# Kernel optimization log

Hardware: AMD Instinct MI355X
Metric: run time of the kernel (lower is better)

The kernel has to match this reference:

```python
import jax, jax.numpy as jnp
import numpy as np

B, H, W, C, NH, WS, SHIFT = 32, 56, 56, 128, 4, 7, 3
N = WS * WS            # tokens per window = 49
HD = C // NH           # head dim = 32
HID = int(C * 4.0)     # mlp hidden = 512
SCALE = HD ** -0.5
EPS = 1e-5


def _rel_index():
    coords = np.stack(np.meshgrid(np.arange(WS), np.arange(WS), indexing='ij')).reshape(2, -1)
    rel = (coords[:, :, None] - coords[:, None, :]).transpose(1, 2, 0).copy()
    rel[:, :, 0] += WS - 1
    rel[:, :, 1] += WS - 1
    rel[:, :, 0] *= 2 * WS - 1
    return jnp.asarray(rel.sum(-1), jnp.int32)  # [N, N]


def setup_inputs() -> dict:
    key = jax.random.key(0)
    ks = jax.random.split(key, 8)
    n = lambda k, s, std=0.02: jax.random.normal(k, s, jnp.float32) * std
    return {
        'x': jax.random.normal(ks[0], (B, H * W, C), jnp.float32),
        'attn_mask': jnp.zeros(((H // WS) * (W // WS), N, N), jnp.float32),  # unused (source bug)
        'norm1_w': jnp.ones((C,), jnp.float32), 'norm1_b': jnp.zeros((C,), jnp.float32),
        'qkv_w': n(ks[1], (3 * C, C)), 'qkv_b': jnp.zeros((3 * C,), jnp.float32),
        'rel_table': n(ks[2], ((2 * WS - 1) ** 2, NH)),
        'rel_index': _rel_index(),
        'proj_w': n(ks[3], (C, C)), 'proj_b': jnp.zeros((C,), jnp.float32),
        'norm2_w': jnp.ones((C,), jnp.float32), 'norm2_b': jnp.zeros((C,), jnp.float32),
        'fc1_w': n(ks[4], (HID, C)), 'fc1_b': jnp.zeros((HID,), jnp.float32),
        'fc2_w': n(ks[5], (C, HID)), 'fc2_b': jnp.zeros((C,), jnp.float32),
    }


def _ln(x, w, b):
    m = x.mean(-1, keepdims=True)
    v = jnp.mean((x - m) ** 2, -1, keepdims=True)
    return (x - m) * jax.lax.rsqrt(v + EPS) * w + b


def reference(x, attn_mask, norm1_w, norm1_b, qkv_w, qkv_b, rel_table, rel_index,
              proj_w, proj_b, norm2_w, norm2_b, fc1_w, fc1_b, fc2_w, fc2_b):
    # NOTE: attn_mask is accepted but never used by the source WindowAttention (faithful).
    shortcut = x
    h = _ln(x, norm1_w, norm1_b).reshape(B, H, W, C)
    # cyclic shift (shift_size > 0)
    h = jnp.roll(h, (-SHIFT, -SHIFT), axis=(1, 2))
    # window partition -> [B*nW, N, C]
    h = h.reshape(B, H // WS, WS, W // WS, WS, C).transpose(0, 1, 3, 2, 4, 5).reshape(-1, N, C)
    # window attention
    qkv = (h @ qkv_w.T + qkv_b).reshape(-1, N, 3, NH, HD)
    q = qkv[:, :, 0].transpose(0, 2, 1, 3)  # [BW, NH, N, HD]
    k = qkv[:, :, 1].transpose(0, 2, 1, 3)
    v = qkv[:, :, 2].transpose(0, 2, 1, 3)
    attn = jnp.einsum('whnd,whmd->whnm', q, k) * SCALE  # [BW, NH, N, N]
    bias = rel_table[rel_index.reshape(-1)].reshape(N, N, NH).transpose(2, 0, 1)
    attn = jax.nn.softmax(attn + bias[None], axis=-1)
    out = jnp.einsum('whnm,whmd->whnd', attn, v).transpose(0, 2, 1, 3).reshape(-1, N, C)
    out = out @ proj_w.T + proj_b
    # window reverse -> [B, H, W, C]
    out = out.reshape(B, H // WS, W // WS, WS, WS, C).transpose(0, 1, 3, 2, 4, 5).reshape(B, H, W, C)
    out = jnp.roll(out, (SHIFT, SHIFT), axis=(1, 2)).reshape(B, H * W, C)
    y = shortcut + out
    # MLP block
    h2 = _ln(y, norm2_w, norm2_b)
    h2 = jax.nn.gelu(h2 @ fc1_w.T + fc1_b, approximate=False)
    h2 = h2 @ fc2_w.T + fc2_b
    return y + h2
```

## Files before the change

### kernel.cpp

```cpp
#include <hip/hip_runtime.h>

typedef __bf16 bf16;
typedef __bf16 bf16x4 __attribute__((ext_vector_type(4)));
typedef __bf16 bf16x8 __attribute__((ext_vector_type(8)));
typedef float f32x4 __attribute__((ext_vector_type(4)));

#define NTOK 49
#define HW 56
#define SHIFT3 3
constexpr float kScale = 0.17677669529663687f;

#define WS_BIAS  0
#define WS_QKVW  50176
#define WS_PROJW 148480
#define WS_FC1W  181248
#define WS_FC2W  312320

static __device__ __forceinline__ f32x4 mfma16(bf16x8 a, bf16x8 b, f32x4 c) {
    return __builtin_amdgcn_mfma_f32_16x16x32_bf16(a, b, c, 0, 0, 0);
}

static __device__ __forceinline__ float gelu_f(float x) {
    float x2 = x * x;
    float u2 = x * (1.5957691216f + 0.0713548162f * x2);
    return x / (1.0f + __expf(-u2));
}


__global__ void bias_kernel(const float* __restrict__ rel_table,
                            const int* __restrict__ rel_index,
                            float* __restrict__ biasbuf) {
    int idx = blockIdx.x * 256 + threadIdx.x;
    if (idx >= 4 * NTOK * 64) return;
    int j = idx & 63;
    int rest = idx >> 6;
    int i = rest % NTOK;
    int h = rest / NTOK;
    float v = -1e30f;
    if (j < NTOK) v = rel_table[rel_index[i * NTOK + j] * 4 + h];
    biasbuf[idx] = v;
}

__global__ void wcvt_kernel(const float* __restrict__ qkv_w, const float* __restrict__ proj_w,
                            const float* __restrict__ fc1_w, const float* __restrict__ fc2_w,
                            bf16* __restrict__ qkvwp, bf16* __restrict__ projwp,
                            bf16* __restrict__ fc1wp, bf16* __restrict__ fc2wp) {
    int idx = blockIdx.x * 256 + threadIdx.x;
    if (idx < 49152) {
        int o = idx, e = o & 7, t = o >> 3, g = t & 3; t >>= 2;
        int row = t % 384, ks = t / 384;
        qkvwp[o] = (bf16)qkv_w[row * 128 + ks * 32 + g * 8 + e];
    } else if (idx < 65536) {
        int o = idx - 49152, e = o & 7, t = o >> 3, g = t & 3; t >>= 2;
        int row = t % 128, ks = t / 128;
        projwp[o] = (bf16)proj_w[row * 128 + ks * 32 + g * 8 + e];
    } else if (idx < 131072) {
        int o = idx - 65536, e = o & 7, t = o >> 3, g = t & 3; t >>= 2;
        int row = t % 512, ks = t / 512;
        fc1wp[o] = (bf16)fc1_w[row * 128 + ks * 32 + g * 8 + e];
    } else {
        int o = idx - 131072, e = o & 7, t = o >> 3, g = t & 3; t >>= 2;
        int row = t % 128, ks = t / 128;
        fc2wp[o] = (bf16)fc2_w[row * 512 + ks * 32 + g * 8 + e];
    }
}


__global__ __launch_bounds__(256, 3) void attn_kernel(
    const float* __restrict__ x,
    const float* __restrict__ n1w, const float* __restrict__ n1b,
    const bf16*  __restrict__ qkvwp, const float* __restrict__ qkv_b,
    const bf16*  __restrict__ projwp, const float* __restrict__ proj_b,
    const float* __restrict__ biasbuf,
    float* __restrict__ yout)
{
    __shared__ __align__(16) char smem[49152];
    bf16* const hb = (bf16*)smem;

    const int tid  = threadIdx.x;
    const int wave = tid >> 6;
    const int lane = tid & 63;
    const int g = lane >> 4;
    const int c = lane & 15;

    char* const qbase  = smem + 16384 + wave * 8192;
    char* const kbase  = qbase + 4096;
    char* const pbase  = qbase;
    char* const vtbase = smem + wave * 4096;

    const int w  = blockIdx.x;
    const int b  = w >> 6;
    const int wi = (w >> 3) & 7;
    const int wj = w & 7;
    const int head = wave;

    {
        const int slot = tid >> 5, l32 = tid & 31;
        for (int it = 0; it < 8; ++it) {
            int t  = slot + (it << 3);
            int tt = t < NTOK ? t : NTOK - 1;
            int r  = tt / 7, cc = tt - r * 7;
            int row = wi * 7 + r + SHIFT3;  if (row >= HW) row -= HW;
            int col = wj * 7 + cc + SHIFT3; if (col >= HW) col -= HW;
            const float* src = x + (((size_t)(b * 3136 + row * 56 + col)) << 7) + (l32 << 2);
            float4 v = *(const float4*)src;
            float s  = v.x + v.y + v.z + v.w;
            float s2 = v.x * v.x + v.y * v.y + v.z * v.z + v.w * v.w;
            for (int m = 1; m <= 16; m <<= 1) {
                s  += __shfl_xor(s,  m, 64);
                s2 += __shfl_xor(s2, m, 64);
            }
            float mean = s * (1.0f / 128.0f);
            float var  = s2 * (1.0f / 128.0f) - mean * mean;
            float rs   = rsqrtf(var + 1e-5f);
            float4 wv = *(const float4*)(n1w + (l32 << 2));
            float4 bv = *(const float4*)(n1b + (l32 << 2));
            bf16x4 outv;
            if (t < NTOK) {
                outv[0] = (bf16)((v.x - mean) * rs * wv.x + bv.x);
                outv[1] = (bf16)((v.y - mean) * rs * wv.y + bv.y);
                outv[2] = (bf16)((v.z - mean) * rs * wv.z + bv.z);
                outv[3] = (bf16)((v.w - mean) * rs * wv.w + bv.w);
            } else {
                outv[0] = (bf16)0.0f; outv[1] = (bf16)0.0f;
                outv[2] = (bf16)0.0f; outv[3] = (bf16)0.0f;
            }
            int off = (l32 << 3) ^ ((t & 7) << 4);
            *(bf16x4*)((char*)hb + t * 256 + off) = outv;
        }
    }
    __syncthreads();

    f32x4 fz = {0.f, 0.f, 0.f, 0.f};
    f32x4 va[2][4];
    #pragma unroll
    for (int nt = 0; nt < 2; ++nt) {
        f32x4 qa[4], ka[4];
        #pragma unroll
        for (int mt = 0; mt < 4; ++mt) { qa[mt] = fz; ka[mt] = fz; va[nt][mt] = fz; }

        #pragma unroll
        for (int ks = 0; ks < 4; ++ks) {
            bf16x8 af[4];
            const int koff = ks * 64 + g * 16;
            #pragma unroll
            for (int mt = 0; mt < 4; ++mt) {
                int row = mt * 16 + c;
                af[mt] = *(const bf16x8*)((char*)hb + row * 256 + (koff ^ ((row & 7) << 4)));
            }
            int jb = head * 32 + nt * 16 + c;
            bf16x8 bq = *(const bf16x8*)(qkvwp + (((ks * 384 + jb) * 4 + g) << 3));
            bf16x8 bk = *(const bf16x8*)(qkvwp + (((ks * 384 + 128 + jb) * 4 + g) << 3));
            bf16x8 bv = *(const bf16x8*)(qkvwp + (((ks * 384 + 256 + jb) * 4 + g) << 3));
            #pragma unroll
            for (int mt = 0; mt < 4; ++mt) {
                qa[mt] = mfma16(bq, af[mt], qa[mt]);
                ka[mt] = mfma16(bk, af[mt], ka[mt]);
                va[nt][mt] = mfma16(af[mt], bv, va[nt][mt]);
            }
        }
        f32x4 qb4 = *(const f32x4*)(qkv_b + head * 32 + nt * 16 + g * 4);
        f32x4 kb4 = *(const f32x4*)(qkv_b + 128 + head * 32 + nt * 16 + g * 4);
        #pragma unroll
        for (int mt = 0; mt < 4; ++mt) {
            int tok = mt * 16 + c;
            bf16x4 qv, kv;
            #pragma unroll
            for (int r = 0; r < 4; ++r) {
                qv[r] = (bf16)(qa[mt][r] + qb4[r]);
                kv[r] = (bf16)(ka[mt][r] + kb4[r]);
            }
            int qoff = (nt * 32 + g * 8) ^ ((tok & 3) << 4);
            *(bf16x4*)(qbase + tok * 64 + qoff) = qv;
            *(bf16x4*)(kbase + tok * 64 + qoff) = kv;
        }
    }
    __syncthreads();

    #pragma unroll
    for (int nt = 0; nt < 2; ++nt) {
        float vb = qkv_b[256 + head * 32 + nt * 16 + c];
        int dl = nt * 16 + c;
        #pragma unroll
        for (int mt = 0; mt < 4; ++mt) {
            bf16x4 vv;
            #pragma unroll
            for (int r = 0; r < 4; ++r) vv[r] = (bf16)(va[nt][mt][r] + vb);
            *(bf16x4*)(vtbase + dl * 128 + ((mt * 32 + g * 8) ^ ((dl & 7) << 4))) = vv;
        }
    }

    f32x4 s[4][4];
    #pragma unroll
    for (int bm = 0; bm < 4; ++bm) for (int bn = 0; bn < 4; ++bn) s[bm][bn] = fz;
    {
        bf16x8 aq[4];
        #pragma unroll
        for (int bm = 0; bm < 4; ++bm) {
            int row = bm * 16 + c;
            aq[bm] = *(const bf16x8*)(qbase + row * 64 + ((g * 16) ^ ((row & 3) << 4)));
        }
        #pragma unroll
        for (int bn = 0; bn < 4; ++bn) {
            int row = bn * 16 + c;
            bf16x8 kf = *(const bf16x8*)(kbase + row * 64 + ((g * 16) ^ ((row & 3) << 4)));
            #pragma unroll
            for (int bm = 0; bm < 4; ++bm) s[bm][bn] = mfma16(kf, aq[bm], s[bm][bn]);
        }
    }

    const float* bbase = biasbuf + head * (NTOK * 64);
    float linv[4];
    #pragma unroll
    for (int bm = 0; bm < 4; ++bm) {
        int qt = bm * 16 + c;
        int im = qt < NTOK ? qt : NTOK - 1;
        const float* brow = bbase + im * 64;
        f32x4 vals[4];
        float mx = -3e38f;
        #pragma unroll
        for (int bn = 0; bn < 4; ++bn) {
            f32x4 b4 = *(const f32x4*)(brow + bn * 16 + g * 4);
            #pragma unroll
            for (int r = 0; r < 4; ++r) {
                float v = s[bm][bn][r] * kScale + b4[r];
                vals[bn][r] = v;
                mx = fmaxf(mx, v);
            }
        }
        mx = fmaxf(mx, __shfl_xor(mx, 16, 64));
        mx = fmaxf(mx, __shfl_xor(mx, 32, 64));
        float sum = 0.f;
        #pragma unroll
        for (int bn = 0; bn < 4; ++bn) {
            bf16x4 pv;
            #pragma unroll
            for (int r = 0; r < 4; ++r) {
                float p = __expf(vals[bn][r] - mx);
                sum += p;
                pv[r] = (bf16)p;
            }
            *(bf16x4*)(pbase + qt * 128 + ((bn * 32 + g * 8) ^ ((c & 7) << 4))) = pv;
        }
        sum += __shfl_xor(sum, 16, 64);
        sum += __shfl_xor(sum, 32, 64);
        linv[bm] = 1.0f / sum;
    }

    f32x4 o[4][2];
    #pragma unroll
    for (int mt = 0; mt < 4; ++mt) for (int nt = 0; nt < 2; ++nt) o[mt][nt] = fz;
    #pragma unroll
    for (int ks = 0; ks < 2; ++ks) {
        int koff = ks * 64 + g * 16;
        bf16x8 vf[2], pf[4];
        #pragma unroll
        for (int nt = 0; nt < 2; ++nt)
            vf[nt] = *(const bf16x8*)(vtbase + (nt * 16 + c) * 128 + (koff ^ ((c & 7) << 4)));
        #pragma unroll
        for (int mt = 0; mt < 4; ++mt)
            pf[mt] = *(const bf16x8*)(pbase + (mt * 16 + c) * 128 + (koff ^ ((c & 7) << 4)));
        #pragma unroll
        for (int mt = 0; mt < 4; ++mt)
            #pragma unroll
            for (int nt = 0; nt < 2; ++nt) o[mt][nt] = mfma16(vf[nt], pf[mt], o[mt][nt]);
    }
    __syncthreads();

    #pragma unroll
    for (int mt = 0; mt < 4; ++mt) {
        int qt = mt * 16 + c;
        if (qt < NTOK) {
            float inv = linv[mt];
            #pragma unroll
            for (int nt = 0; nt < 2; ++nt) {
                bf16x4 ov;
                #pragma unroll
                for (int r = 0; r < 4; ++r) ov[r] = (bf16)(o[mt][nt][r] * inv);
                int coff = (head * 64 + nt * 32 + g * 8) ^ ((qt & 7) << 4);
                *(bf16x4*)((char*)hb + qt * 256 + coff) = ov;
            }
        }
    }
    __syncthreads();

    f32x4 pj[4][2];
    #pragma unroll
    for (int mt = 0; mt < 4; ++mt) for (int nt = 0; nt < 2; ++nt) pj[mt][nt] = fz;
    #pragma unroll
    for (int ks = 0; ks < 4; ++ks) {
        bf16x8 af[4];
        int koff = ks * 64 + g * 16;
        #pragma unroll
        for (int mt = 0; mt < 4; ++mt) {
            int row = mt * 16 + c;
            af[mt] = *(const bf16x8*)((char*)hb + row * 256 + (koff ^ ((row & 7) << 4)));
        }
        #pragma unroll
        for (int nt = 0; nt < 2; ++nt) {
            int colw = wave * 32 + nt * 16 + c;
            bf16x8 bp = *(const bf16x8*)(projwp + (((ks * 128 + colw) * 4 + g) << 3));
            #pragma unroll
            for (int mt = 0; mt < 4; ++mt) pj[mt][nt] = mfma16(bp, af[mt], pj[mt][nt]);
        }
    }
    f32x4 pb0 = *(const f32x4*)(proj_b + wave * 32 + g * 4);
    f32x4 pb1 = *(const f32x4*)(proj_b + wave * 32 + 16 + g * 4);
    #pragma unroll
    for (int mt = 0; mt < 4; ++mt) {
        int qt = mt * 16 + c;
        if (qt < NTOK) {
            int rr = qt / 7, cc = qt - rr * 7;
            int row = wi * 7 + rr + SHIFT3;  if (row >= HW) row -= HW;
            int col = wj * 7 + cc + SHIFT3;  if (col >= HW) col -= HW;
            size_t base = ((size_t)(b * 3136 + row * 56 + col)) << 7;
            int c0 = wave * 32 + g * 4;
            f32x4 x0 = *(const f32x4*)(x + base + c0);
            f32x4 x1 = *(const f32x4*)(x + base + c0 + 16);
            f32x4 y0 = x0 + pj[mt][0] + pb0;
            f32x4 y1 = x1 + pj[mt][1] + pb1;
            *(f32x4*)(yout + base + c0)      = y0;
            *(f32x4*)(yout + base + c0 + 16) = y1;
        }
    }
}


__global__ __launch_bounds__(256, 5) void mlp_kernel(
    const float* __restrict__ n2w, const float* __restrict__ n2b,
    const bf16*  __restrict__ fc1wp, const float* __restrict__ fc1_b,
    const bf16*  __restrict__ fc2wp, const float* __restrict__ fc2_b,
    float* __restrict__ y)
{
    __shared__ __align__(16) char smem[32768];
    bf16* const h2    = (bf16*)smem;
    char* const abase = smem;

    const int tid  = threadIdx.x;
    const int wave = tid >> 6;
    const int lane = tid & 63;
    const int g = lane >> 4;
    const int c = lane & 15;
    const size_t t0 = (size_t)blockIdx.x * 32;

    {
        const int slot = tid >> 5, l32 = tid & 31;
        for (int it = 0; it < 4; ++it) {
            int t = slot + (it << 3);
            const float* src = y + ((t0 + t) << 7) + (l32 << 2);
            float4 v = *(const float4*)src;
            float s  = v.x + v.y + v.z + v.w;
            float s2 = v.x * v.x + v.y * v.y + v.z * v.z + v.w * v.w;
            for (int m = 1; m <= 16; m <<= 1) {
                s  += __shfl_xor(s,  m, 64);
                s2 += __shfl_xor(s2, m, 64);
            }
            float mean = s * (1.0f / 128.0f);
            float var  = s2 * (1.0f / 128.0f) - mean * mean;
            float rs   = rsqrtf(var + 1e-5f);
            float4 wv = *(const float4*)(n2w + (l32 << 2));
            float4 bv = *(const float4*)(n2b + (l32 << 2));
            bf16x4 outv;
            outv[0] = (bf16)((v.x - mean) * rs * wv.x + bv.x);
            outv[1] = (bf16)((v.y - mean) * rs * wv.y + bv.y);
            outv[2] = (bf16)((v.z - mean) * rs * wv.z + bv.z);
            outv[3] = (bf16)((v.w - mean) * rs * wv.w + bv.w);
            int off = (l32 << 3) ^ ((t & 7) << 4);
            *(bf16x4*)((char*)h2 + t * 256 + off) = outv;
        }
    }
    __syncthreads();

    f32x4 fz = {0.f, 0.f, 0.f, 0.f};
    f32x4 a1[8][2];
    #pragma unroll
    for (int nt = 0; nt < 8; ++nt) for (int mt = 0; mt < 2; ++mt) a1[nt][mt] = fz;
    #pragma unroll
    for (int ks = 0; ks < 4; ++ks) {
        bf16x8 af[2];
        int koff = ks * 64 + g * 16;
        #pragma unroll
        for (int mt = 0; mt < 2; ++mt) {
            int row = mt * 16 + c;
            af[mt] = *(const bf16x8*)((char*)h2 + row * 256 + (koff ^ ((row & 7) << 4)));
        }
        #pragma unroll
        for (int nt = 0; nt < 8; ++nt) {
            int col = wave * 128 + nt * 16 + c;
            bf16x8 bw = *(const bf16x8*)(fc1wp + (((ks * 512 + col) * 4 + g) << 3));
            #pragma unroll
            for (int mt = 0; mt < 2; ++mt) a1[nt][mt] = mfma16(bw, af[mt], a1[nt][mt]);
        }
    }
    __syncthreads();

    #pragma unroll
    for (int nt = 0; nt < 8; ++nt) {
        f32x4 fb4 = *(const f32x4*)(fc1_b + wave * 128 + nt * 16 + g * 4);
        #pragma unroll
        for (int mt = 0; mt < 2; ++mt) {
            int tok = mt * 16 + c;
            bf16x4 gv;
            #pragma unroll
            for (int r = 0; r < 4; ++r) gv[r] = (bf16)gelu_f(a1[nt][mt][r] + fb4[r]);
            int coff = (wave * 256 + nt * 32 + g * 8) ^ ((tok & 7) << 4);
            *(bf16x4*)(abase + tok * 1024 + coff) = gv;
        }
    }
    __syncthreads();

    f32x4 a2[2][2];
    #pragma unroll
    for (int nt = 0; nt < 2; ++nt) for (int mt = 0; mt < 2; ++mt) a2[nt][mt] = fz;
    #pragma unroll 4
    for (int ks = 0; ks < 16; ++ks) {
        bf16x8 af[2];
        int koff = ks * 64 + g * 16;
        #pragma unroll
        for (int mt = 0; mt < 2; ++mt) {
            int row = mt * 16 + c;
            af[mt] = *(const bf16x8*)(abase + row * 1024 + (koff ^ ((row & 7) << 4)));
        }
        #pragma unroll
        for (int nt = 0; nt < 2; ++nt) {
            int col = wave * 32 + nt * 16 + c;
            bf16x8 bw = *(const bf16x8*)(fc2wp + (((ks * 128 + col) * 4 + g) << 3));
            #pragma unroll
            for (int mt = 0; mt < 2; ++mt) a2[nt][mt] = mfma16(bw, af[mt], a2[nt][mt]);
        }
    }
    #pragma unroll
    for (int nt = 0; nt < 2; ++nt) {
        f32x4 fb4 = *(const f32x4*)(fc2_b + wave * 32 + nt * 16 + g * 4);
        #pragma unroll
        for (int mt = 0; mt < 2; ++mt) {
            size_t idx = ((t0 + mt * 16 + c) << 7) + wave * 32 + nt * 16 + g * 4;
            f32x4 yv = *(const f32x4*)(y + idx);
            yv = yv + a2[nt][mt] + fb4;
            *(f32x4*)(y + idx) = yv;
        }
    }
}


extern "C" void kernel_launch(void* const* d_in, const int* in_sizes, int n_in,
                              void* d_out, int out_size, void* d_ws, size_t ws_size,
                              hipStream_t stream) {
    const float* x        = (const float*)d_in[0];
    const float* n1w      = (const float*)d_in[2];
    const float* n1b      = (const float*)d_in[3];
    const float* qkv_w    = (const float*)d_in[4];
    const float* qkv_b    = (const float*)d_in[5];
    const float* rel_tab  = (const float*)d_in[6];
    const int*   rel_idx  = (const int*)d_in[7];
    const float* proj_w   = (const float*)d_in[8];
    const float* proj_b   = (const float*)d_in[9];
    const float* n2w      = (const float*)d_in[10];
    const float* n2b      = (const float*)d_in[11];
    const float* fc1_w    = (const float*)d_in[12];
    const float* fc1_b    = (const float*)d_in[13];
    const float* fc2_w    = (const float*)d_in[14];
    const float* fc2_b    = (const float*)d_in[15];

    float* yout = (float*)d_out;
    char*  ws   = (char*)d_ws;
    float* biasbuf = (float*)(ws + WS_BIAS);
    bf16*  qkvwp = (bf16*)(ws + WS_QKVW);
    bf16*  projwp= (bf16*)(ws + WS_PROJW);
    bf16*  fc1wp = (bf16*)(ws + WS_FC1W);
    bf16*  fc2wp = (bf16*)(ws + WS_FC2W);

    bias_kernel<<<dim3(49), dim3(256), 0, stream>>>(rel_tab, rel_idx, biasbuf);
    wcvt_kernel<<<dim3(768), dim3(256), 0, stream>>>(qkv_w, proj_w, fc1_w, fc2_w,
                                                     qkvwp, projwp, fc1wp, fc2wp);
    attn_kernel<<<dim3(2048), dim3(256), 0, stream>>>(x, n1w, n1b, qkvwp, qkv_b,
                                                      projwp, proj_b, biasbuf, yout);
    mlp_kernel<<<dim3(3136), dim3(256), 0, stream>>>(n2w, n2b, fc1wp, fc1_b,
                                                     fc2wp, fc2_b, yout);
}
```

Measured before the change: 279.7 us.

## Fuse MLP block into window-attention kernel, keeping residual in registers

Merges the MLP kernel into the attention kernel. The post-projection residual stays in registers, LayerNorm2 is done with a cross-wave reduction through shared memory, and fc1/GELU/fc2 run in two hidden-dimension chunks that reuse shared memory. This removes the fp32 y round trip through global memory and one kernel launch. In exchange the fused kernel has higher register pressure, extra barriers, and M-tiles padded to 64 rows for 49 tokens, which wastes MFMA work in the MLP.

```diff
diff --git a/kernel.cpp b/kernel.cpp
--- a/kernel.cpp
+++ b/kernel.cpp
@@ -66,12 +66,15 @@
 }
 
 
-__global__ __launch_bounds__(256, 3) void attn_kernel(
+__global__ __launch_bounds__(256, 3) void attn_mlp_kernel(
     const float* __restrict__ x,
     const float* __restrict__ n1w, const float* __restrict__ n1b,
     const bf16*  __restrict__ qkvwp, const float* __restrict__ qkv_b,
     const bf16*  __restrict__ projwp, const float* __restrict__ proj_b,
     const float* __restrict__ biasbuf,
+    const float* __restrict__ n2w, const float* __restrict__ n2b,
+    const bf16*  __restrict__ fc1wp, const float* __restrict__ fc1_b,
+    const bf16*  __restrict__ fc2wp, const float* __restrict__ fc2_b,
     float* __restrict__ yout)
 {
     __shared__ __align__(16) char smem[49152];
@@ -87,6 +90,7 @@
     char* const kbase  = qbase + 4096;
     char* const pbase  = qbase;
     char* const vtbase = smem + wave * 4096;
+    char* const abase  = smem + 16384;
 
     const int w  = blockIdx.x;
     const int b  = w >> 6;
@@ -306,6 +310,7 @@
     }
     f32x4 pb0 = *(const f32x4*)(proj_b + wave * 32 + g * 4);
     f32x4 pb1 = *(const f32x4*)(proj_b + wave * 32 + 16 + g * 4);
+    f32x4 yreg[4][2];
     #pragma unroll
     for (int mt = 0; mt < 4; ++mt) {
         int qt = mt * 16 + c;
@@ -317,127 +322,144 @@
             int c0 = wave * 32 + g * 4;
             f32x4 x0 = *(const f32x4*)(x + base + c0);
             f32x4 x1 = *(const f32x4*)(x + base + c0 + 16);
-            f32x4 y0 = x0 + pj[mt][0] + pb0;
-            f32x4 y1 = x1 + pj[mt][1] + pb1;
-            *(f32x4*)(yout + base + c0)      = y0;
-            *(f32x4*)(yout + base + c0 + 16) = y1;
-        }
-    }
-}
-
-
-__global__ __launch_bounds__(256, 5) void mlp_kernel(
-    const float* __restrict__ n2w, const float* __restrict__ n2b,
-    const bf16*  __restrict__ fc1wp, const float* __restrict__ fc1_b,
-    const bf16*  __restrict__ fc2wp, const float* __restrict__ fc2_b,
-    float* __restrict__ y)
-{
-    __shared__ __align__(16) char smem[32768];
-    bf16* const h2    = (bf16*)smem;
-    char* const abase = smem;
-
-    const int tid  = threadIdx.x;
-    const int wave = tid >> 6;
-    const int lane = tid & 63;
-    const int g = lane >> 4;
-    const int c = lane & 15;
-    const size_t t0 = (size_t)blockIdx.x * 32;
+            yreg[mt][0] = x0 + pj[mt][0] + pb0;
+            yreg[mt][1] = x1 + pj[mt][1] + pb1;
+        } else {
+            yreg[mt][0] = fz; yreg[mt][1] = fz;
+        }
+    }
 
     {
-        const int slot = tid >> 5, l32 = tid & 31;
-        for (int it = 0; it < 4; ++it) {
-            int t = slot + (it << 3);
-            const float* src = y + ((t0 + t) << 7) + (l32 << 2);
-            float4 v = *(const float4*)src;
-            float s  = v.x + v.y + v.z + v.w;
-            float s2 = v.x * v.x + v.y * v.y + v.z * v.z + v.w * v.w;
-            for (int m = 1; m <= 16; m <<= 1) {
-                s  += __shfl_xor(s,  m, 64);
-                s2 += __shfl_xor(s2, m, 64);
-            }
-            float mean = s * (1.0f / 128.0f);
-            float var  = s2 * (1.0f / 128.0f) - mean * mean;
-            float rs   = rsqrtf(var + 1e-5f);
-            float4 wv = *(const float4*)(n2w + (l32 << 2));
-            float4 bv = *(const float4*)(n2b + (l32 << 2));
-            bf16x4 outv;
-            outv[0] = (bf16)((v.x - mean) * rs * wv.x + bv.x);
-            outv[1] = (bf16)((v.y - mean) * rs * wv.y + bv.y);
-            outv[2] = (bf16)((v.z - mean) * rs * wv.z + bv.z);
-            outv[3] = (bf16)((v.w - mean) * rs * wv.w + bv.w);
-            int off = (l32 << 3) ^ ((t & 7) << 4);
-            *(bf16x4*)((char*)h2 + t * 256 + off) = outv;
+        float* ssum = (float*)(smem + 16384);
+        float* ssq  = (float*)(smem + 16384 + 1024);
+        float lns[4], lnq[4];
+        #pragma unroll
+        for (int mt = 0; mt < 4; ++mt) {
+            float ps = 0.f, pq = 0.f;
+            #pragma unroll
+            for (int nt = 0; nt < 2; ++nt)
+                #pragma unroll
+                for (int r = 0; r < 4; ++r) {
+                    float v = yreg[mt][nt][r];
+                    ps += v; pq += v * v;
+                }
+            ps += __shfl_xor(ps, 16, 64);  pq += __shfl_xor(pq, 16, 64);
+            ps += __shfl_xor(ps, 32, 64);  pq += __shfl_xor(pq, 32, 64);
+            lns[mt] = ps; lnq[mt] = pq;
+        }
+        if (g == 0) {
+            #pragma unroll
+            for (int mt = 0; mt < 4; ++mt) {
+                int tok = mt * 16 + c;
+                ssum[tok * 4 + wave] = lns[mt];
+                ssq [tok * 4 + wave] = lnq[mt];
+            }
+        }
+        __syncthreads();
+
+        #pragma unroll
+        for (int mt = 0; mt < 4; ++mt) {
+            int tok = mt * 16 + c;
+            f32x4 s4 = *(const f32x4*)(ssum + tok * 4);
+            f32x4 q4 = *(const f32x4*)(ssq  + tok * 4);
+            float sm = s4[0] + s4[1] + s4[2] + s4[3];
+            float sq = q4[0] + q4[1] + q4[2] + q4[3];
+            float mean = sm * (1.0f / 128.0f);
+            float var  = sq * (1.0f / 128.0f) - mean * mean;
+            float rsv  = rsqrtf(var + 1e-5f);
+            #pragma unroll
+            for (int nt = 0; nt < 2; ++nt) {
+                int ch = wave * 32 + nt * 16 + g * 4;
+                f32x4 w4 = *(const f32x4*)(n2w + ch);
+                f32x4 b4 = *(const f32x4*)(n2b + ch);
+                bf16x4 hv;
+                #pragma unroll
+                for (int r = 0; r < 4; ++r)
+                    hv[r] = (bf16)((yreg[mt][nt][r] - mean) * rsv * w4[r] + b4[r]);
+                *(bf16x4*)((char*)hb + tok * 256 + ((ch * 2) ^ ((tok & 7) << 4))) = hv;
+            }
         }
     }
     __syncthreads();
 
-    f32x4 fz = {0.f, 0.f, 0.f, 0.f};
-    f32x4 a1[8][2];
-    #pragma unroll
-    for (int nt = 0; nt < 8; ++nt) for (int mt = 0; mt < 2; ++mt) a1[nt][mt] = fz;
-    #pragma unroll
-    for (int ks = 0; ks < 4; ++ks) {
-        bf16x8 af[2];
-        int koff = ks * 64 + g * 16;
-        #pragma unroll
-        for (int mt = 0; mt < 2; ++mt) {
-            int row = mt * 16 + c;
-            af[mt] = *(const bf16x8*)((char*)h2 + row * 256 + (koff ^ ((row & 7) << 4)));
-        }
-        #pragma unroll
-        for (int nt = 0; nt < 8; ++nt) {
-            int col = wave * 128 + nt * 16 + c;
-            bf16x8 bw = *(const bf16x8*)(fc1wp + (((ks * 512 + col) * 4 + g) << 3));
-            #pragma unroll
-            for (int mt = 0; mt < 2; ++mt) a1[nt][mt] = mfma16(bw, af[mt], a1[nt][mt]);
-        }
-    }
-    __syncthreads();
-
-    #pragma unroll
-    for (int nt = 0; nt < 8; ++nt) {
-        f32x4 fb4 = *(const f32x4*)(fc1_b + wave * 128 + nt * 16 + g * 4);
-        #pragma unroll
-        for (int mt = 0; mt < 2; ++mt) {
-            int tok = mt * 16 + c;
-            bf16x4 gv;
-            #pragma unroll
-            for (int r = 0; r < 4; ++r) gv[r] = (bf16)gelu_f(a1[nt][mt][r] + fb4[r]);
-            int coff = (wave * 256 + nt * 32 + g * 8) ^ ((tok & 7) << 4);
-            *(bf16x4*)(abase + tok * 1024 + coff) = gv;
-        }
-    }
-    __syncthreads();
-
-    f32x4 a2[2][2];
-    #pragma unroll
-    for (int nt = 0; nt < 2; ++nt) for (int mt = 0; mt < 2; ++mt) a2[nt][mt] = fz;
-    #pragma unroll 4
-    for (int ks = 0; ks < 16; ++ks) {
-        bf16x8 af[2];
-        int koff = ks * 64 + g * 16;
-        #pragma unroll
-        for (int mt = 0; mt < 2; ++mt) {
-            int row = mt * 16 + c;
-            af[mt] = *(const bf16x8*)(abase + row * 1024 + (koff ^ ((row & 7) << 4)));
-        }
-        #pragma unroll
-        for (int nt = 0; nt < 2; ++nt) {
-            int col = wave * 32 + nt * 16 + c;
-            bf16x8 bw = *(const bf16x8*)(fc2wp + (((ks * 128 + col) * 4 + g) << 3));
-            #pragma unroll
-            for (int mt = 0; mt < 2; ++mt) a2[nt][mt] = mfma16(bw, af[mt], a2[nt][mt]);
-        }
-    }
-    #pragma unroll
-    for (int nt = 0; nt < 2; ++nt) {
-        f32x4 fb4 = *(const f32x4*)(fc2_b + wave * 32 + nt * 16 + g * 4);
-        #pragma unroll
-        for (int mt = 0; mt < 2; ++mt) {
-            size_t idx = ((t0 + mt * 16 + c) << 7) + wave * 32 + nt * 16 + g * 4;
-            f32x4 yv = *(const f32x4*)(y + idx);
-            yv = yv + a2[nt][mt] + fb4;
-            *(f32x4*)(y + idx) = yv;
+    f32x4 a2acc[2][4];
+    #pragma unroll
+    for (int nt = 0; nt < 2; ++nt) for (int mt = 0; mt < 4; ++mt) a2acc[nt][mt] = fz;
+
+    #pragma unroll 1
+    for (int p = 0; p < 2; ++p) {
+        #pragma unroll 1
+        for (int sub = 0; sub < 2; ++sub) {
+            f32x4 t1[2][4];
+            #pragma unroll
+            for (int nt = 0; nt < 2; ++nt) for (int mt = 0; mt < 4; ++mt) t1[nt][mt] = fz;
+            #pragma unroll
+            for (int ks = 0; ks < 4; ++ks) {
+                bf16x8 af[4];
+                int koff = ks * 64 + g * 16;
+                #pragma unroll
+                for (int mt = 0; mt < 4; ++mt) {
+                    int row = mt * 16 + c;
+                    af[mt] = *(const bf16x8*)((char*)hb + row * 256 + (koff ^ ((row & 7) << 4)));
+                }
+                #pragma unroll
+                for (int nt = 0; nt < 2; ++nt) {
+                    int col = p * 256 + wave * 64 + sub * 32 + nt * 16 + c;
+                    bf16x8 bw = *(const bf16x8*)(fc1wp + (((ks * 512 + col) * 4 + g) << 3));
+                    #pragma unroll
+                    for (int mt = 0; mt < 4; ++mt) t1[nt][mt] = mfma16(bw, af[mt], t1[nt][mt]);
+                }
+            }
+            #pragma unroll
+            for (int nt = 0; nt < 2; ++nt) {
+                f32x4 fb4 = *(const f32x4*)(fc1_b + p * 256 + wave * 64 + sub * 32 + nt * 16 + g * 4);
+                int hloc2 = (wave * 64 + sub * 32 + nt * 16 + g * 4) * 2;
+                #pragma unroll
+                for (int mt = 0; mt < 4; ++mt) {
+                    int tok = mt * 16 + c;
+                    bf16x4 gv;
+                    #pragma unroll
+                    for (int r = 0; r < 4; ++r) gv[r] = (bf16)gelu_f(t1[nt][mt][r] + fb4[r]);
+                    *(bf16x4*)(abase + tok * 512 + (hloc2 ^ ((tok & 7) << 4))) = gv;
+                }
+            }
+        }
+        __syncthreads();
+        #pragma unroll
+        for (int ks2 = 0; ks2 < 8; ++ks2) {
+            bf16x8 af2[4];
+            int koff = ks2 * 64 + g * 16;
+            #pragma unroll
+            for (int mt = 0; mt < 4; ++mt) {
+                int row = mt * 16 + c;
+                af2[mt] = *(const bf16x8*)(abase + row * 512 + (koff ^ ((row & 7) << 4)));
+            }
+            int gks = p * 8 + ks2;
+            #pragma unroll
+            for (int nt = 0; nt < 2; ++nt) {
+                int col = wave * 32 + nt * 16 + c;
+                bf16x8 bw = *(const bf16x8*)(fc2wp + (((gks * 128 + col) * 4 + g) << 3));
+                #pragma unroll
+                for (int mt = 0; mt < 4; ++mt) a2acc[nt][mt] = mfma16(bw, af2[mt], a2acc[nt][mt]);
+            }
+        }
+        __syncthreads();
+    }
+
+    #pragma unroll
+    for (int mt = 0; mt < 4; ++mt) {
+        int qt = mt * 16 + c;
+        if (qt < NTOK) {
+            int rr = qt / 7, cc = qt - rr * 7;
+            int row = wi * 7 + rr + SHIFT3;  if (row >= HW) row -= HW;
+            int col = wj * 7 + cc + SHIFT3;  if (col >= HW) col -= HW;
+            size_t base = ((size_t)(b * 3136 + row * 56 + col)) << 7;
+            #pragma unroll
+            for (int nt = 0; nt < 2; ++nt) {
+                f32x4 fb4 = *(const f32x4*)(fc2_b + wave * 32 + nt * 16 + g * 4);
+                f32x4 out = yreg[mt][nt] + a2acc[nt][mt] + fb4;
+                *(f32x4*)(yout + base + wave * 32 + nt * 16 + g * 4) = out;
+            }
         }
     }
 }
@@ -473,8 +495,7 @@
     bias_kernel<<<dim3(49), dim3(256), 0, stream>>>(rel_tab, rel_idx, biasbuf);
     wcvt_kernel<<<dim3(768), dim3(256), 0, stream>>>(qkv_w, proj_w, fc1_w, fc2_w,
                                                      qkvwp, projwp, fc1wp, fc2wp);
-    attn_kernel<<<dim3(2048), dim3(256), 0, stream>>>(x, n1w, n1b, qkvwp, qkv_b,
-                                                      projwp, proj_b, biasbuf, yout);
-    mlp_kernel<<<dim3(3136), dim3(256), 0, stream>>>(n2w, n2b, fc1wp, fc1_b,
-                                                     fc2wp, fc2_b, yout);
+    attn_mlp_kernel<<<dim3(2048), dim3(256), 0, stream>>>(
+        x, n1w, n1b, qkvwp, qkv_b, projwp, proj_b, biasbuf,
+        n2w, n2b, fc1wp, fc1_b, fc2wp, fc2_b, yout);
 }
```

Result: faster. 242.0 us (-13.5%).
